# Performance work log

Measured on AMD Instinct MI355X. Metric: run time of the kernel, lower is better.

Reference implementation:

```python
import jax, jax.numpy as jnp
import numpy as np

N, E, IN, HID, ADIM, EDIM, H = 20000, 320000, 128, 128, 16, 16, 2


def _lin(key, out_d, in_d, scale=0.05):
    kw, kb = jax.random.split(key)
    W = jax.random.normal(kw, (out_d, in_d), jnp.float32) * scale
    b = jax.random.normal(kb, (out_d,), jnp.float32) * scale
    return W, b


def _gat_params(key):
    k = jax.random.split(key, 4)
    Wl, bl = _lin(k[0], H * HID, HID)
    Wr, br = _lin(k[1], H * HID, HID)
    We = jax.random.normal(k[2], (H * HID, EDIM), jnp.float32) * 0.05  # lin_edge, no bias
    att = jax.random.normal(k[3], (1, H, HID), jnp.float32) * 0.05
    bias = jnp.zeros((HID,), jnp.float32)  # concat=False -> out bias of size HID
    return Wl, bl, Wr, br, We, att, bias


def setup_inputs() -> dict:
    key = jax.random.key(0)
    ks = jax.random.split(key, 16)
    inp = {}
    inp['x'] = jax.random.normal(ks[0], (N, IN), jnp.float32)
    inp['edge_index'] = jax.random.randint(ks[1], (2, E), 0, N, jnp.int64 if jax.config.jax_enable_x64 else jnp.int32)
    inp['edge_attr'] = jax.random.normal(ks[2], (E, EDIM), jnp.float32)
    inp['action'] = jax.random.normal(ks[3], (N, ADIM), jnp.float32)
    inp['inp_W'], inp['inp_b'] = _lin(ks[4], HID, IN)
    for i, name in enumerate(['s1', 's2', 'sa']):
        Wl, bl, Wr, br, We, att, bias = _gat_params(ks[5 + i])
        inp[f'{name}_Wl'], inp[f'{name}_bl'] = Wl, bl
        inp[f'{name}_Wr'], inp[f'{name}_br'] = Wr, br
        inp[f'{name}_We'], inp[f'{name}_att'], inp[f'{name}_bias'] = We, att, bias
    inp['ap_W'], inp['ap_b'] = _lin(ks[8], HID, ADIM)
    inp['g_W'], inp['g_b'] = _lin(ks[9], HID, HID)
    inp['be_W'], inp['be_b'] = _lin(ks[10], HID, HID)
    inp['q1_W'], inp['q1_b'] = _lin(ks[11], HID, HID)
    inp['q2_W'], inp['q2_b'] = _lin(ks[12], 1, HID)
    return inp


def gatv2(h, src, dst, ea, Wl, bl, Wr, br, We, att, bias):
    """PyG GATv2Conv, heads=H, concat=False (mean over heads), with edge_attr."""
    n = h.shape[0]
    xl = (h @ Wl.T + bl).reshape(n, H, HID)   # source transform
    xr = (h @ Wr.T + br).reshape(n, H, HID)   # destination transform
    em = (ea @ We.T).reshape(-1, H, HID)      # [E,H,C]
    m = jax.nn.leaky_relu(xl[src] + xr[dst] + em, 0.2)   # [E,H,C]
    logit = (m * att).sum(-1)                 # [E,H]
    lmax = jax.ops.segment_max(logit, dst, num_segments=n)
    w = jnp.exp(logit - lmax[dst])
    den = jax.ops.segment_sum(w, dst, num_segments=n)
    alpha = w / den[dst]                      # segment softmax over incoming edges
    out = jax.ops.segment_sum(alpha[..., None] * xl[src], dst, num_segments=n)  # [n,H,C]
    return out.mean(axis=1) + bias


def reference(x, edge_index, edge_attr, action, inp_W, inp_b,
              s1_Wl, s1_bl, s1_Wr, s1_br, s1_We, s1_att, s1_bias,
              s2_Wl, s2_bl, s2_Wr, s2_br, s2_We, s2_att, s2_bias,
              sa_Wl, sa_bl, sa_Wr, sa_br, sa_We, sa_att, sa_bias,
              ap_W, ap_b, g_W, g_b, be_W, be_b, q1_W, q1_b, q2_W, q2_b):
    src, dst = edge_index[0], edge_index[1]
    h = jax.nn.relu(x @ inp_W.T + inp_b)
    h = jax.nn.relu(gatv2(h, src, dst, edge_attr, s1_Wl, s1_bl, s1_Wr, s1_br, s1_We, s1_att, s1_bias))
    h = jax.nn.relu(gatv2(h, src, dst, edge_attr, s2_Wl, s2_bl, s2_Wr, s2_br, s2_We, s2_att, s2_bias))
    a = jax.nn.relu(action @ ap_W.T + ap_b)
    h = (a @ g_W.T + g_b) * h + (a @ be_W.T + be_b)   # FiLM modulation
    h = jax.nn.relu(gatv2(h, src, dst, edge_attr, sa_Wl, sa_bl, sa_Wr, sa_br, sa_We, sa_att, sa_bias))
    h = jax.nn.relu(h @ q1_W.T + q1_b)
    q_node = h @ q2_W.T + q2_b                         # [N,1]
    return q_node.mean(axis=0, keepdims=True)          # [1,1]
```

## Files before the change

### kernel.cpp

```cpp
#include <hip/hip_runtime.h>
#include <hip/hip_bf16.h>


typedef __attribute__((ext_vector_type(8))) short bf16x8;
typedef __attribute__((ext_vector_type(4))) float f32x4;
typedef __attribute__((ext_vector_type(2))) float f32x2;

#define ZERO8 ((bf16x8){0, 0, 0, 0, 0, 0, 0, 0})

__device__ __forceinline__ unsigned short f2bf(float f) {
    union { float f; unsigned int i; } v; v.f = f;
    unsigned int x = v.i;
    x += 0x7fffu + ((x >> 16) & 1u);
    return (unsigned short)(x >> 16);
}
__device__ __forceinline__ unsigned char f2fp8(float f) {
    return (unsigned char)(__builtin_amdgcn_cvt_pk_fp8_f32(f, f, 0, false) & 0xFF);
}
__device__ __forceinline__ void wave_lds_fence() {
    __builtin_amdgcn_wave_barrier();
    asm volatile("s_waitcnt lgkmcnt(0)" ::: "memory");
    __builtin_amdgcn_wave_barrier();
}

#define MAXCVT 16
struct CvtDescs {
    const float* src[MAXCVT];
    unsigned short* dst[MAXCVT];
    int off4[MAXCVT + 1];
    int cnt;
    int* deg; int ndeg4;
    int* ctr; float* col;
};
__global__ __launch_bounds__(256) void cvt_many_kernel(CvtDescs d) {
    const int tid = blockIdx.x * blockDim.x + threadIdx.x;
    const int stride = gridDim.x * blockDim.x;
    const int total = d.off4[d.cnt];
    for (int i = tid; i < total; i += stride) {
        int e = 0;
        while (d.off4[e + 1] <= i) ++e;
        const int j = i - d.off4[e];
        float4 v = ((const float4*)d.src[e])[j];
        ((ushort4*)d.dst[e])[j] = make_ushort4(f2bf(v.x), f2bf(v.y), f2bf(v.z), f2bf(v.w));
    }
    for (int i = tid; i < d.ndeg4; i += stride)
        ((int4*)d.deg)[i] = make_int4(0, 0, 0, 0);
    if (tid == 0) { *d.ctr = 0; *d.col = 0.f; }
}

__global__ void hist_kernel(const int* __restrict__ dst, int* __restrict__ deg, int n) {
    int i = blockIdx.x * blockDim.x + threadIdx.x;
    if (i < n) atomicAdd(&deg[dst[i]], 1);
}

__global__ __launch_bounds__(1024) void scan_kernel(const int* __restrict__ deg,
                                                    int* __restrict__ rowp,
                                                    int* __restrict__ cur, int n) {
    __shared__ int sums[1024];
    const int t = threadIdx.x;
    const int PER = 20;
    int base = t * PER;
    int local[PER];
    int run = 0;
#pragma unroll
    for (int i = 0; i < PER; ++i) {
        int v = (base + i < n) ? deg[base + i] : 0;
        local[i] = run; run += v;
    }
    sums[t] = run; __syncthreads();
    for (int off = 1; off < 1024; off <<= 1) {
        int v = (t >= off) ? sums[t - off] : 0;
        __syncthreads();
        sums[t] += v;
        __syncthreads();
    }
    int offs = (t > 0) ? sums[t - 1] : 0;
#pragma unroll
    for (int i = 0; i < PER; ++i) {
        int idx = base + i;
        if (idx < n) { int v = offs + local[i]; rowp[idx] = v; cur[idx] = v; }
    }
    if (t == 0) rowp[n] = sums[1023];
}

__global__ void scatter_kernel(const int* __restrict__ src, const int* __restrict__ dst,
                               int* __restrict__ cur, const float4* __restrict__ ea,
                               int* __restrict__ csrs, int* __restrict__ csrd,
                               ushort4* __restrict__ eacsr, int n) {
    int i = blockIdx.x * blockDim.x + threadIdx.x;
    if (i < n) {
        int d = dst[i];
        int p = atomicAdd(&cur[d], 1);
        csrs[p] = src[i];
        csrd[p] = d;
        const float4* er = ea + (size_t)i * 4;
        ushort4* eo = eacsr + (size_t)p * 4;
#pragma unroll
        for (int q = 0; q < 4; ++q) {
            float4 v = er[q];
            eo[q] = make_ushort4(f2bf(v.x), f2bf(v.y), f2bf(v.z), f2bf(v.w));
        }
    }
}

template <bool RELU, bool SPLIT, bool AF32>
__global__ __launch_bounds__(256) void gemm_mfma_kernel(
    const void* __restrict__ Ap, const unsigned short* __restrict__ W,
    const float* __restrict__ bias0, const float* __restrict__ bias1, int bsplit,
    unsigned short* __restrict__ Cbf, unsigned char* __restrict__ Cf8,
    int M, int N, int K) {
    __shared__ unsigned char ctile[SPLIT ? 128 * 64 : 64];
    const int t = threadIdx.x;
    const int wave = t >> 6, lane = t & 63;
    const int lo = lane & 15, quad = lane >> 4;
    const int m0 = blockIdx.y * 128 + wave * 32;
    const int n0 = blockIdx.x * 64;

    f32x4 acc[2][4];
#pragma unroll
    for (int i = 0; i < 2; ++i)
#pragma unroll
        for (int j = 0; j < 4; ++j) acc[i][j] = (f32x4){0.f, 0.f, 0.f, 0.f};

    for (int k0 = 0; k0 < K; k0 += 32) {
        bf16x8 af[2], bfr[4];
#pragma unroll
        for (int mi = 0; mi < 2; ++mi) {
            const int mb = m0 + mi * 16;
            if (mb >= M) { af[mi] = ZERO8; continue; }
            if (AF32) {
                const float* A = (const float*)Ap;
                float4 a0 = *(const float4*)(A + (size_t)(mb + lo) * K + k0 + quad * 8);
                float4 a1 = *(const float4*)(A + (size_t)(mb + lo) * K + k0 + quad * 8 + 4);
                bf16x8 f;
                f[0] = (short)f2bf(a0.x); f[1] = (short)f2bf(a0.y);
                f[2] = (short)f2bf(a0.z); f[3] = (short)f2bf(a0.w);
                f[4] = (short)f2bf(a1.x); f[5] = (short)f2bf(a1.y);
                f[6] = (short)f2bf(a1.z); f[7] = (short)f2bf(a1.w);
                af[mi] = f;
            } else {
                const unsigned short* A = (const unsigned short*)Ap;
                af[mi] = *(const bf16x8*)(A + (size_t)(mb + lo) * K + k0 + quad * 8);
            }
        }
#pragma unroll
        for (int ni = 0; ni < 4; ++ni)
            bfr[ni] = *(const bf16x8*)(W + (size_t)(n0 + ni * 16 + lo) * K + k0 + quad * 8);
#pragma unroll
        for (int mi = 0; mi < 2; ++mi)
#pragma unroll
            for (int ni = 0; ni < 4; ++ni)
                acc[mi][ni] = __builtin_amdgcn_mfma_f32_16x16x32_bf16(af[mi], bfr[ni], acc[mi][ni], 0, 0, 0);
    }

    float bn[4];
#pragma unroll
    for (int ni = 0; ni < 4; ++ni) {
        const int n = n0 + ni * 16 + lo;
        const float* bp = (n < bsplit) ? bias0 : bias1;
        const int bi = (n < bsplit) ? n : n - bsplit;
        bn[ni] = bp[bi];
    }
    if (SPLIT) {
#pragma unroll
        for (int mi = 0; mi < 2; ++mi) {
#pragma unroll
            for (int ni = 0; ni < 4; ++ni) {
                const int n = ni * 16 + lo;
#pragma unroll
                for (int r = 0; r < 4; ++r) {
                    float o = acc[mi][ni][r] + bn[ni];
                    if (RELU) o = fmaxf(o, 0.f);
                    ctile[(wave * 32 + mi * 16 + quad * 4 + r) * 64 + n] = f2fp8(o);
                }
            }
        }
        __syncthreads();
        const int row = t >> 1, half = t & 1;
        const int grow = blockIdx.y * 128 + row;
        if (grow < M) {
            const unsigned char* srcp = &ctile[row * 64 + half * 32];
            unsigned char* dstp = Cf8 + (size_t)grow * 512 + n0 + half * 32;
            *(int4*)(dstp) = *(const int4*)(srcp);
            *(int4*)(dstp + 16) = *(const int4*)(srcp + 16);
        }
    } else {
#pragma unroll
        for (int mi = 0; mi < 2; ++mi) {
            const int mb = m0 + mi * 16;
            if (mb >= M) continue;
#pragma unroll
            for (int ni = 0; ni < 4; ++ni) {
                const int n = n0 + ni * 16 + lo;
#pragma unroll
                for (int r = 0; r < 4; ++r) {
                    float o = acc[mi][ni][r] + bn[ni];
                    if (RELU) o = fmaxf(o, 0.f);
                    Cbf[(size_t)(mb + quad * 4 + r) * N + n] = f2bf(o);
                }
            }
        }
    }
}

__global__ __launch_bounds__(256) void gemm_film_kernel(
    const unsigned short* __restrict__ A, const unsigned short* __restrict__ Wg,
    const unsigned short* __restrict__ Wb, const float* __restrict__ gb,
    const float* __restrict__ bb, unsigned short* __restrict__ hbf, int M) {
    const int K = 128, N = 128;
    const int t = threadIdx.x;
    const int wave = t >> 6, lane = t & 63;
    const int lo = lane & 15, quad = lane >> 4;
    const int m0 = blockIdx.y * 128 + wave * 32;
    const int n0 = blockIdx.x * 64;

    f32x4 accg[2][4], accb[2][4];
#pragma unroll
    for (int i = 0; i < 2; ++i)
#pragma unroll
        for (int j = 0; j < 4; ++j) { accg[i][j] = (f32x4){0.f,0.f,0.f,0.f}; accb[i][j] = accg[i][j]; }

    for (int k0 = 0; k0 < 128; k0 += 32) {
        bf16x8 af[2], bg4[4];
#pragma unroll
        for (int mi = 0; mi < 2; ++mi) {
            const int mb = m0 + mi * 16;
            af[mi] = (mb < M) ? *(const bf16x8*)(A + (size_t)(mb + lo) * K + k0 + quad * 8)
                              : ZERO8;
        }
#pragma unroll
        for (int ni = 0; ni < 4; ++ni)
            bg4[ni] = *(const bf16x8*)(Wg + (size_t)(n0 + ni * 16 + lo) * K + k0 + quad * 8);
#pragma unroll
        for (int mi = 0; mi < 2; ++mi)
#pragma unroll
            for (int ni = 0; ni < 4; ++ni)
                accg[mi][ni] = __builtin_amdgcn_mfma_f32_16x16x32_bf16(af[mi], bg4[ni], accg[mi][ni], 0, 0, 0);
#pragma unroll
        for (int ni = 0; ni < 4; ++ni)
            bg4[ni] = *(const bf16x8*)(Wb + (size_t)(n0 + ni * 16 + lo) * K + k0 + quad * 8);
#pragma unroll
        for (int mi = 0; mi < 2; ++mi)
#pragma unroll
            for (int ni = 0; ni < 4; ++ni)
                accb[mi][ni] = __builtin_amdgcn_mfma_f32_16x16x32_bf16(af[mi], bg4[ni], accb[mi][ni], 0, 0, 0);
    }

#pragma unroll
    for (int mi = 0; mi < 2; ++mi) {
        const int mb = m0 + mi * 16;
        if (mb >= M) continue;
#pragma unroll
        for (int ni = 0; ni < 4; ++ni) {
            const int n = n0 + ni * 16 + lo;
            const float g = gb[n], b = bb[n];
#pragma unroll
            for (int r = 0; r < 4; ++r) {
                const size_t idx = (size_t)(mb + quad * 4 + r) * N + n;
                union { unsigned int i; float f; } hv; hv.i = (unsigned int)hbf[idx] << 16;
                hbf[idx] = f2bf((accg[mi][ni][r] + g) * hv.f + (accb[mi][ni][r] + b));
            }
        }
    }
}

__global__ __launch_bounds__(256) void gemm_q1_kernel(
    const unsigned short* __restrict__ A, const unsigned short* __restrict__ W,
    const float* __restrict__ q1b, const float* __restrict__ q2w,
    const float* __restrict__ q2b, float* __restrict__ outsum,
    float* __restrict__ outv, int* __restrict__ ctr,
    int M, int nblk, float invn) {
    const int K = 128;
    const int t = threadIdx.x;
    const int wave = t >> 6, lane = t & 63;
    const int lo = lane & 15, quad = lane >> 4;
    const int m0 = blockIdx.y * 128 + wave * 32;
    const int n0 = blockIdx.x * 64;
    __shared__ float red[4];

    f32x4 acc[2][4];
#pragma unroll
    for (int i = 0; i < 2; ++i)
#pragma unroll
        for (int j = 0; j < 4; ++j) acc[i][j] = (f32x4){0.f, 0.f, 0.f, 0.f};

    for (int k0 = 0; k0 < K; k0 += 32) {
        bf16x8 af[2], bfr[4];
#pragma unroll
        for (int mi = 0; mi < 2; ++mi) {
            const int mb = m0 + mi * 16;
            af[mi] = (mb < M) ? *(const bf16x8*)(A + (size_t)(mb + lo) * K + k0 + quad * 8)
                              : ZERO8;
        }
#pragma unroll
        for (int ni = 0; ni < 4; ++ni)
            bfr[ni] = *(const bf16x8*)(W + (size_t)(n0 + ni * 16 + lo) * K + k0 + quad * 8);
#pragma unroll
        for (int mi = 0; mi < 2; ++mi)
#pragma unroll
            for (int ni = 0; ni < 4; ++ni)
                acc[mi][ni] = __builtin_amdgcn_mfma_f32_16x16x32_bf16(af[mi], bfr[ni], acc[mi][ni], 0, 0, 0);
    }

    float partial = 0.f;
#pragma unroll
    for (int mi = 0; mi < 2; ++mi) {
        const int mb = m0 + mi * 16;
        if (mb >= M) continue;
#pragma unroll
        for (int ni = 0; ni < 4; ++ni) {
            const int n = n0 + ni * 16 + lo;
            const float b = q1b[n], w = q2w[n];
#pragma unroll
            for (int r = 0; r < 4; ++r)
                partial += fmaxf(acc[mi][ni][r] + b, 0.f) * w;
        }
    }
    partial += __shfl_xor(partial, 1);  partial += __shfl_xor(partial, 2);
    partial += __shfl_xor(partial, 4);  partial += __shfl_xor(partial, 8);
    partial += __shfl_xor(partial, 16); partial += __shfl_xor(partial, 32);
    if (lane == 0) red[wave] = partial;
    __syncthreads();
    if (t == 0) {
        atomicAdd(outsum, red[0] + red[1] + red[2] + red[3]);
        __threadfence();
        unsigned int d = atomicAdd((unsigned int*)ctr, 1u);
        if (d == (unsigned int)(nblk - 1)) {
            float s = atomicAdd(outsum, 0.f);
            outv[0] = s * invn + q2b[0];
        }
    }
}

template <int BK, bool RELU>
__global__ __launch_bounds__(256) void gemm_kernel(const float* __restrict__ A,
                                                   const float* __restrict__ W,
                                                   const float* __restrict__ bp,
                                                   unsigned short* __restrict__ Cbf,
                                                   int M, int N, int K) {
    __shared__ float As[BK][68];
    __shared__ float Ws[BK][68];
    const int t = threadIdx.x;
    const int m0 = blockIdx.y * 64;
    const int n0 = blockIdx.x * 64;
    const int tx = t & 15, ty = t >> 4;
    float acc[4][4];
#pragma unroll
    for (int i = 0; i < 4; ++i)
#pragma unroll
        for (int j = 0; j < 4; ++j) acc[i][j] = 0.f;

    for (int k0 = 0; k0 < K; k0 += BK) {
        const int r = t >> 2, cc = (t & 3) * 4;
        const int arow = m0 + r;
        float4 av = (arow < M) ? *(const float4*)(A + (size_t)arow * K + k0 + cc)
                               : make_float4(0.f, 0.f, 0.f, 0.f);
        As[cc + 0][r] = av.x; As[cc + 1][r] = av.y;
        As[cc + 2][r] = av.z; As[cc + 3][r] = av.w;
        float4 wv = *(const float4*)(W + (size_t)(n0 + r) * K + k0 + cc);
        Ws[cc + 0][r] = wv.x; Ws[cc + 1][r] = wv.y;
        Ws[cc + 2][r] = wv.z; Ws[cc + 3][r] = wv.w;
        __syncthreads();
#pragma unroll
        for (int k = 0; k < BK; ++k) {
            float4 a4 = *(const float4*)&As[k][ty * 4];
            float4 b4 = *(const float4*)&Ws[k][tx * 4];
            float a_[4] = {a4.x, a4.y, a4.z, a4.w};
            float b_[4] = {b4.x, b4.y, b4.z, b4.w};
#pragma unroll
            for (int i = 0; i < 4; ++i)
#pragma unroll
                for (int j = 0; j < 4; ++j) acc[i][j] += a_[i] * b_[j];
        }
        __syncthreads();
    }
    float4 bj = *(const float4*)(bp + n0 + tx * 4);
    float bb[4] = {bj.x, bj.y, bj.z, bj.w};
#pragma unroll
    for (int i = 0; i < 4; ++i) {
        int row = m0 + ty * 4 + i;
        if (row < M) {
            float o[4];
#pragma unroll
            for (int j = 0; j < 4; ++j) {
                o[j] = acc[i][j] + bb[j];
                if (RELU) o[j] = fmaxf(o[j], 0.f);
            }
            *(ushort4*)(Cbf + (size_t)row * N + n0 + tx * 4) =
                make_ushort4(f2bf(o[0]), f2bf(o[1]), f2bf(o[2]), f2bf(o[3]));
        }
    }
}

#define LSTR 272
__global__ __launch_bounds__(256, 4) void gat_logit_kernel(
    const unsigned char* __restrict__ xf8,
    const int* __restrict__ csrs, const int* __restrict__ csrd,
    const unsigned short* __restrict__ eacsr, const unsigned short* __restrict__ we16,
    const float* __restrict__ att, float* __restrict__ logit, int E) {
    __shared__ float attl[256];
    __shared__ __align__(16) unsigned char xls[4][16 * LSTR];
    __shared__ __align__(16) unsigned char xrs[4][16 * LSTR];
    const int tid = threadIdx.x;
    attl[tid] = att[tid];
    const int wave = tid >> 6, lane = tid & 63;
    const int lo = lane & 15, quad = lane >> 4;
    const int sr_row = lane >> 2, c16 = (lane & 3) * 16;

    bf16x8 wef[16];
#pragma unroll
    for (int t = 0; t < 16; ++t)
        wef[t] = (quad < 2) ? *(const bf16x8*)(we16 + (size_t)(t * 16 + lo) * 16 + quad * 8)
                            : ZERO8;
    __syncthreads();

    const int nb = (E + 15) / 16;
    const int wstride = gridDim.x * 4;
    const int trips = (nb + wstride - 1) / wstride;
    for (int it = 0; it < trips; ++it) {
        const int b = blockIdx.x * 4 + wave + it * wstride;
        if (b >= nb) break;
        const int p0 = b * 16;
        {
            const int pr = min(p0 + sr_row, E - 1);
            const int sr = csrs[pr], dr = csrd[pr];
            const unsigned char* xs = xf8 + (size_t)sr * 512 + c16;
            const unsigned char* xrp = xf8 + (size_t)dr * 512 + 256 + c16;
            unsigned char* ld = &xls[wave][sr_row * LSTR + c16];
            unsigned char* rd = &xrs[wave][sr_row * LSTR + c16];
#pragma unroll
            for (int j = 0; j < 4; ++j) {
                *(int4*)(ld + j * 64) = *(const int4*)(xs + j * 64);
                *(int4*)(rd + j * 64) = *(const int4*)(xrp + j * 64);
            }
        }
        wave_lds_fence();
        {
            const bool valid = (p0 + lo) < E;
            const int p = valid ? (p0 + lo) : (E - 1);
            const bf16x8 eaf = (quad < 2)
                ? *(const bf16x8*)(eacsr + (size_t)p * 16 + quad * 8) : ZERO8;
            float ph0 = 0.f, ph1 = 0.f;
#pragma unroll
            for (int t = 0; t < 16; ++t) {
                f32x4 D = __builtin_amdgcn_mfma_f32_16x16x32_bf16(
                    wef[t], eaf, (f32x4){0.f, 0.f, 0.f, 0.f}, 0, 0, 0);
                const int c0 = t * 16 + quad * 4;
                const unsigned int xlu = *(const unsigned int*)&xls[wave][lo * LSTR + c0];
                const unsigned int xru = *(const unsigned int*)&xrs[wave][lo * LSTR + c0];
                const f32x2 l01 = __builtin_amdgcn_cvt_pk_f32_fp8(xlu, false);
                const f32x2 l23 = __builtin_amdgcn_cvt_pk_f32_fp8(xlu, true);
                const f32x2 r01 = __builtin_amdgcn_cvt_pk_f32_fp8(xru, false);
                const f32x2 r23 = __builtin_amdgcn_cvt_pk_f32_fp8(xru, true);
                const float4 at4 = *(const float4*)&attl[c0];
                float vx = l01.x + r01.x + D[0];
                float vy = l01.y + r01.y + D[1];
                float vz = l23.x + r23.x + D[2];
                float vw = l23.y + r23.y + D[3];
                vx = fmaxf(vx, 0.2f * vx); vy = fmaxf(vy, 0.2f * vy);
                vz = fmaxf(vz, 0.2f * vz); vw = fmaxf(vw, 0.2f * vw);
                const float pt = vx * at4.x + vy * at4.y + vz * at4.z + vw * at4.w;
                if (t < 8) ph0 += pt; else ph1 += pt;
            }
            ph0 += __shfl_xor(ph0, 16); ph0 += __shfl_xor(ph0, 32);
            ph1 += __shfl_xor(ph1, 16); ph1 += __shfl_xor(ph1, 32);
            if (valid) {
                if (quad == 0) logit[p0 + lo] = __expf(fminf(ph0, 60.f));
                else if (quad == 1) logit[(size_t)E + p0 + lo] = __expf(fminf(ph1, 60.f));
            }
        }
        wave_lds_fence();
    }
}

__global__ __launch_bounds__(256) void gat_na_kernel(
    const unsigned char* __restrict__ xf8,
    const int* __restrict__ rowp, const int* __restrict__ csrs,
    const float* __restrict__ wgt, const float* __restrict__ bias,
    unsigned short* __restrict__ houtb, int nnodes, int E) {
    const int lane = threadIdx.x & 63;
    const int node = blockIdx.x * 4 + (threadIdx.x >> 6);
    if (node >= nnodes) return;
    const int rs = rowp[node], re = rowp[node + 1];
    const int h = lane >> 5;
    const float* lg = wgt + (size_t)h * E;

    float den = 0.f;
    float4 acc = make_float4(0.f, 0.f, 0.f, 0.f);
    int i = rs;
    for (; i + 3 < re; i += 4) {
        const int s0 = csrs[i], s1 = csrs[i + 1], s2 = csrs[i + 2], s3 = csrs[i + 3];
        const float w0 = lg[i], w1 = lg[i + 1], w2 = lg[i + 2], w3 = lg[i + 3];
        const unsigned int u0 = *(const unsigned int*)(xf8 + (size_t)s0 * 512 + 4 * lane);
        const unsigned int u1 = *(const unsigned int*)(xf8 + (size_t)s1 * 512 + 4 * lane);
        const unsigned int u2 = *(const unsigned int*)(xf8 + (size_t)s2 * 512 + 4 * lane);
        const unsigned int u3 = *(const unsigned int*)(xf8 + (size_t)s3 * 512 + 4 * lane);
        den += (w0 + w1) + (w2 + w3);
        f32x2 p01, p23;
        p01 = __builtin_amdgcn_cvt_pk_f32_fp8(u0, false);
        p23 = __builtin_amdgcn_cvt_pk_f32_fp8(u0, true);
        acc.x += w0 * p01.x; acc.y += w0 * p01.y; acc.z += w0 * p23.x; acc.w += w0 * p23.y;
        p01 = __builtin_amdgcn_cvt_pk_f32_fp8(u1, false);
        p23 = __builtin_amdgcn_cvt_pk_f32_fp8(u1, true);
        acc.x += w1 * p01.x; acc.y += w1 * p01.y; acc.z += w1 * p23.x; acc.w += w1 * p23.y;
        p01 = __builtin_amdgcn_cvt_pk_f32_fp8(u2, false);
        p23 = __builtin_amdgcn_cvt_pk_f32_fp8(u2, true);
        acc.x += w2 * p01.x; acc.y += w2 * p01.y; acc.z += w2 * p23.x; acc.w += w2 * p23.y;
        p01 = __builtin_amdgcn_cvt_pk_f32_fp8(u3, false);
        p23 = __builtin_amdgcn_cvt_pk_f32_fp8(u3, true);
        acc.x += w3 * p01.x; acc.y += w3 * p01.y; acc.z += w3 * p23.x; acc.w += w3 * p23.y;
    }
    for (; i < re; ++i) {
        const int s0 = csrs[i];
        const float w0 = lg[i];
        const unsigned int u0 = *(const unsigned int*)(xf8 + (size_t)s0 * 512 + 4 * lane);
        const f32x2 p01 = __builtin_amdgcn_cvt_pk_f32_fp8(u0, false);
        const f32x2 p23 = __builtin_amdgcn_cvt_pk_f32_fp8(u0, true);
        den += w0;
        acc.x += w0 * p01.x; acc.y += w0 * p01.y; acc.z += w0 * p23.x; acc.w += w0 * p23.y;
    }
    const float inv = (re > rs) ? 1.f / den : 0.f;
    float ox = acc.x * inv, oy = acc.y * inv, oz = acc.z * inv, ow = acc.w * inv;
    ox += __shfl_xor(ox, 32); oy += __shfl_xor(oy, 32);
    oz += __shfl_xor(oz, 32); ow += __shfl_xor(ow, 32);
    if (lane < 32) {
        float4 bu = *(const float4*)(bias + 4 * lane);
        *(ushort4*)(houtb + (size_t)node * 128 + 4 * lane) = make_ushort4(
            f2bf(fmaxf(0.5f * ox + bu.x, 0.f)), f2bf(fmaxf(0.5f * oy + bu.y, 0.f)),
            f2bf(fmaxf(0.5f * oz + bu.z, 0.f)), f2bf(fmaxf(0.5f * ow + bu.w, 0.f)));
    }
}

extern "C" void kernel_launch(void* const* d_in, const int* in_sizes, int n_in,
                              void* d_out, int out_size, void* d_ws, size_t ws_size,
                              hipStream_t stream) {
    const int N = in_sizes[0] / 128;
    const int E = in_sizes[1] / 2;

    typedef const float* fp;
    fp x      = (fp)d_in[0];
    const int* ei = (const int*)d_in[1];
    fp ea     = (fp)d_in[2];
    fp action = (fp)d_in[3];
    fp inp_W  = (fp)d_in[4];
    fp inp_b  = (fp)d_in[5];
    fp ap_W = (fp)d_in[27], ap_b = (fp)d_in[28];
    fp g_W  = (fp)d_in[29], g_b  = (fp)d_in[30];
    fp be_W = (fp)d_in[31], be_b = (fp)d_in[32];
    fp q1_W = (fp)d_in[33], q1_b = (fp)d_in[34];
    fp q2_W = (fp)d_in[35], q2_b = (fp)d_in[36];

    char* base = (char*)d_ws;
    size_t off = 0;
    auto alloc = [&](size_t bytes) { char* p = base + off; off = (off + bytes + 255) & ~(size_t)255; return p; };
    unsigned char*  xf8 = (unsigned char*)alloc((size_t)N * 512);
    float* col  = (float*)alloc(128 * 4);
    int* ctr    = (int*)alloc(256);
    int* deg    = (int*)alloc((size_t)N * 4);
    int* rowp   = (int*)alloc((size_t)(N + 1) * 4);
    int* cur    = (int*)alloc((size_t)N * 4);
    int* csrs   = (int*)alloc((size_t)E * 4);
    int* csrd   = (int*)alloc((size_t)E * 4);
    unsigned short* eacsr = (unsigned short*)alloc((size_t)E * 16 * 2);
    float* wgt  = (float*)alloc((size_t)2 * E * 4);
    unsigned short* hbf = (unsigned short*)alloc((size_t)N * 128 * 2);
    unsigned short* abf = (unsigned short*)alloc((size_t)N * 128 * 2);
    unsigned short* wbf = (unsigned short*)alloc((262144 + 3 * 4096) * 2);
    (void)ws_size; (void)n_in; (void)out_size;

    unsigned short* winp = wbf;
    unsigned short* w1l  = wbf + 16384;
    unsigned short* w1r  = w1l + 32768;
    unsigned short* w2l  = w1r + 32768;
    unsigned short* w2r  = w2l + 32768;
    unsigned short* wal  = w2r + 32768;
    unsigned short* war  = wal + 32768;
    unsigned short* wg   = war + 32768;
    unsigned short* wbe  = wg + 16384;
    unsigned short* wq1  = wbe + 16384;
    unsigned short* wep1 = wq1 + 16384;
    unsigned short* wep2 = wep1 + 4096;
    unsigned short* wep3 = wep2 + 4096;

    const int* src = ei;
    const int* dst = ei + E;

    CvtDescs cd;
    int ce = 0, acc4 = 0;
    auto addc = [&](const float* s, unsigned short* d, int n) {
        cd.src[ce] = s; cd.dst[ce] = d; cd.off4[ce] = acc4; acc4 += n / 4; ++ce; };
    addc(inp_W, winp, 16384);
    addc((fp)d_in[6],  w1l, 32768); addc((fp)d_in[8],  w1r, 32768);
    addc((fp)d_in[13], w2l, 32768); addc((fp)d_in[15], w2r, 32768);
    addc((fp)d_in[20], wal, 32768); addc((fp)d_in[22], war, 32768);
    addc(g_W, wg, 16384); addc(be_W, wbe, 16384); addc(q1_W, wq1, 16384);
    addc((fp)d_in[10], wep1, 4096); addc((fp)d_in[17], wep2, 4096); addc((fp)d_in[24], wep3, 4096);
    cd.off4[ce] = acc4; cd.cnt = ce;
    cd.deg = deg; cd.ndeg4 = (N + 3) / 4;
    cd.ctr = ctr; cd.col = col;
    cvt_many_kernel<<<(acc4 + 255) / 256, 256, 0, stream>>>(cd);

    hist_kernel<<<(E + 255) / 256, 256, 0, stream>>>(dst, deg, E);
    scan_kernel<<<1, 1024, 0, stream>>>(deg, rowp, cur, N);
    scatter_kernel<<<(E + 255) / 256, 256, 0, stream>>>(src, dst, cur, (const float4*)ea,
                                                        csrs, csrd, (ushort4*)eacsr, E);

    const int my = (N + 127) / 128;
    const int nodeg = (N + 3) / 4;

    auto run_gat = [&](const unsigned short* wep, const float* at, const float* bi,
                       unsigned short* hb) {
        gat_logit_kernel<<<2500, 256, 0, stream>>>(xf8, csrs, csrd, eacsr, wep, at, wgt, E);
        gat_na_kernel<<<nodeg, 256, 0, stream>>>(xf8, rowp, csrs, wgt, bi, hb, N, E);
    };

    gemm_mfma_kernel<true, false, true><<<dim3(2, my), 256, 0, stream>>>(
        x, winp, inp_b, inp_b, 128, hbf, nullptr, N, 128, 128);

    gemm_mfma_kernel<false, true, false><<<dim3(8, my), 256, 0, stream>>>(
        hbf, w1l, (fp)d_in[7], (fp)d_in[9], 256, nullptr, xf8, N, 512, 128);
    run_gat(wep1, (fp)d_in[11], (fp)d_in[12], hbf);
    gemm_mfma_kernel<false, true, false><<<dim3(8, my), 256, 0, stream>>>(
        hbf, w2l, (fp)d_in[14], (fp)d_in[16], 256, nullptr, xf8, N, 512, 128);
    run_gat(wep2, (fp)d_in[18], (fp)d_in[19], hbf);

    gemm_kernel<16, true><<<dim3(2, (N + 63) / 64), 256, 0, stream>>>(
        action, ap_W, ap_b, abf, N, 128, 16);
    gemm_film_kernel<<<dim3(2, my), 256, 0, stream>>>(abf, wg, wbe, g_b, be_b, hbf, N);

    gemm_mfma_kernel<false, true, false><<<dim3(8, my), 256, 0, stream>>>(
        hbf, wal, (fp)d_in[21], (fp)d_in[23], 256, nullptr, xf8, N, 512, 128);
    run_gat(wep3, (fp)d_in[25], (fp)d_in[26], hbf);

    gemm_q1_kernel<<<dim3(2, my), 256, 0, stream>>>(
        hbf, wq1, q1_b, q2_W, q2_b, col, (float*)d_out, ctr, N, 2 * my, 1.0f / (float)N);
}
```

Measured before the change: 423.1 us.

## Fuse GATv2 logit and neighbor aggregation into one per-node kernel

Replaces the edge-parallel logit kernel and the node-parallel aggregation kernel with a single kernel in which each wave owns one destination node. It walks that node's CSR edges in chunks of 16, computing the exp-logits with MFMA and reusing the gathered source features already staged in LDS for the weighted sum. The intent is to avoid writing and re-reading the per-edge logit array, to drop the csrd array, to load the destination features once per node instead of per edge, and to gather each source row only once. The trade-offs are wasted MFMA lanes on partial chunks for low-degree nodes, load imbalance across skewed degrees, and reloading the edge-weight fragments in every one of many small blocks.

```diff
diff --git a/kernel.cpp b/kernel.cpp
--- a/kernel.cpp
+++ b/kernel.cpp
@@ -85,14 +85,13 @@
 
 __global__ void scatter_kernel(const int* __restrict__ src, const int* __restrict__ dst,
                                int* __restrict__ cur, const float4* __restrict__ ea,
-                               int* __restrict__ csrs, int* __restrict__ csrd,
+                               int* __restrict__ csrs,
                                ushort4* __restrict__ eacsr, int n) {
     int i = blockIdx.x * blockDim.x + threadIdx.x;
     if (i < n) {
         int d = dst[i];
         int p = atomicAdd(&cur[d], 1);
         csrs[p] = src[i];
-        csrd[p] = d;
         const float4* er = ea + (size_t)i * 4;
         ushort4* eo = eacsr + (size_t)p * 4;
 #pragma unroll
@@ -393,14 +392,16 @@
 }
 
 #define LSTR 272
-__global__ __launch_bounds__(256, 4) void gat_logit_kernel(
+__global__ __launch_bounds__(256, 4) void gat_fused_kernel(
     const unsigned char* __restrict__ xf8,
-    const int* __restrict__ csrs, const int* __restrict__ csrd,
+    const int* __restrict__ rowp, const int* __restrict__ csrs,
     const unsigned short* __restrict__ eacsr, const unsigned short* __restrict__ we16,
-    const float* __restrict__ att, float* __restrict__ logit, int E) {
+    const float* __restrict__ att, const float* __restrict__ bias,
+    unsigned short* __restrict__ houtb, int nnodes) {
     __shared__ float attl[256];
     __shared__ __align__(16) unsigned char xls[4][16 * LSTR];
-    __shared__ __align__(16) unsigned char xrs[4][16 * LSTR];
+    __shared__ __align__(16) unsigned char xrs[4][256];
+    __shared__ float wls[4][2][16];
     const int tid = threadIdx.x;
     attl[tid] = att[tid];
     const int wave = tid >> 6, lane = tid & 63;
@@ -414,30 +415,31 @@
                             : ZERO8;
     __syncthreads();
 
-    const int nb = (E + 15) / 16;
-    const int wstride = gridDim.x * 4;
-    const int trips = (nb + wstride - 1) / wstride;
-    for (int it = 0; it < trips; ++it) {
-        const int b = blockIdx.x * 4 + wave + it * wstride;
-        if (b >= nb) break;
-        const int p0 = b * 16;
+    const int node = blockIdx.x * 4 + wave;
+    if (node >= nnodes) return;
+    const int rs = rowp[node], re = rowp[node + 1];
+
+    *(unsigned int*)&xrs[wave][4 * lane] =
+        *(const unsigned int*)(xf8 + (size_t)node * 512 + 256 + 4 * lane);
+
+    const int h = lane >> 5;
+    float den = 0.f;
+    float4 acc = make_float4(0.f, 0.f, 0.f, 0.f);
+
+    for (int cb = rs; cb < re; cb += 16) {
         {
-            const int pr = min(p0 + sr_row, E - 1);
-            const int sr = csrs[pr], dr = csrd[pr];
+            const int pr = min(cb + sr_row, re - 1);
+            const int sr = csrs[pr];
             const unsigned char* xs = xf8 + (size_t)sr * 512 + c16;
-            const unsigned char* xrp = xf8 + (size_t)dr * 512 + 256 + c16;
             unsigned char* ld = &xls[wave][sr_row * LSTR + c16];
-            unsigned char* rd = &xrs[wave][sr_row * LSTR + c16];
-#pragma unroll
-            for (int j = 0; j < 4; ++j) {
+#pragma unroll
+            for (int j = 0; j < 4; ++j)
                 *(int4*)(ld + j * 64) = *(const int4*)(xs + j * 64);
-                *(int4*)(rd + j * 64) = *(const int4*)(xrp + j * 64);
-            }
         }
         wave_lds_fence();
         {
-            const bool valid = (p0 + lo) < E;
-            const int p = valid ? (p0 + lo) : (E - 1);
+            const bool valid = (cb + lo) < re;
+            const int p = valid ? (cb + lo) : (re - 1);
             const bf16x8 eaf = (quad < 2)
                 ? *(const bf16x8*)(eacsr + (size_t)p * 16 + quad * 8) : ZERO8;
             float ph0 = 0.f, ph1 = 0.f;
@@ -447,7 +449,7 @@
                     wef[t], eaf, (f32x4){0.f, 0.f, 0.f, 0.f}, 0, 0, 0);
                 const int c0 = t * 16 + quad * 4;
                 const unsigned int xlu = *(const unsigned int*)&xls[wave][lo * LSTR + c0];
-                const unsigned int xru = *(const unsigned int*)&xrs[wave][lo * LSTR + c0];
+                const unsigned int xru = *(const unsigned int*)&xrs[wave][c0];
                 const f32x2 l01 = __builtin_amdgcn_cvt_pk_f32_fp8(xlu, false);
                 const f32x2 l23 = __builtin_amdgcn_cvt_pk_f32_fp8(xlu, true);
                 const f32x2 r01 = __builtin_amdgcn_cvt_pk_f32_fp8(xru, false);
@@ -464,61 +466,27 @@
             }
             ph0 += __shfl_xor(ph0, 16); ph0 += __shfl_xor(ph0, 32);
             ph1 += __shfl_xor(ph1, 16); ph1 += __shfl_xor(ph1, 32);
-            if (valid) {
-                if (quad == 0) logit[p0 + lo] = __expf(fminf(ph0, 60.f));
-                else if (quad == 1) logit[(size_t)E + p0 + lo] = __expf(fminf(ph1, 60.f));
+            if (quad == 0) {
+                wls[wave][0][lo] = valid ? __expf(fminf(ph0, 60.f)) : 0.f;
+                wls[wave][1][lo] = valid ? __expf(fminf(ph1, 60.f)) : 0.f;
             }
         }
         wave_lds_fence();
-    }
-}
-
-__global__ __launch_bounds__(256) void gat_na_kernel(
-    const unsigned char* __restrict__ xf8,
-    const int* __restrict__ rowp, const int* __restrict__ csrs,
-    const float* __restrict__ wgt, const float* __restrict__ bias,
-    unsigned short* __restrict__ houtb, int nnodes, int E) {
-    const int lane = threadIdx.x & 63;
-    const int node = blockIdx.x * 4 + (threadIdx.x >> 6);
-    if (node >= nnodes) return;
-    const int rs = rowp[node], re = rowp[node + 1];
-    const int h = lane >> 5;
-    const float* lg = wgt + (size_t)h * E;
-
-    float den = 0.f;
-    float4 acc = make_float4(0.f, 0.f, 0.f, 0.f);
-    int i = rs;
-    for (; i + 3 < re; i += 4) {
-        const int s0 = csrs[i], s1 = csrs[i + 1], s2 = csrs[i + 2], s3 = csrs[i + 3];
-        const float w0 = lg[i], w1 = lg[i + 1], w2 = lg[i + 2], w3 = lg[i + 3];
-        const unsigned int u0 = *(const unsigned int*)(xf8 + (size_t)s0 * 512 + 4 * lane);
-        const unsigned int u1 = *(const unsigned int*)(xf8 + (size_t)s1 * 512 + 4 * lane);
-        const unsigned int u2 = *(const unsigned int*)(xf8 + (size_t)s2 * 512 + 4 * lane);
-        const unsigned int u3 = *(const unsigned int*)(xf8 + (size_t)s3 * 512 + 4 * lane);
-        den += (w0 + w1) + (w2 + w3);
-        f32x2 p01, p23;
-        p01 = __builtin_amdgcn_cvt_pk_f32_fp8(u0, false);
-        p23 = __builtin_amdgcn_cvt_pk_f32_fp8(u0, true);
-        acc.x += w0 * p01.x; acc.y += w0 * p01.y; acc.z += w0 * p23.x; acc.w += w0 * p23.y;
-        p01 = __builtin_amdgcn_cvt_pk_f32_fp8(u1, false);
-        p23 = __builtin_amdgcn_cvt_pk_f32_fp8(u1, true);
-        acc.x += w1 * p01.x; acc.y += w1 * p01.y; acc.z += w1 * p23.x; acc.w += w1 * p23.y;
-        p01 = __builtin_amdgcn_cvt_pk_f32_fp8(u2, false);
-        p23 = __builtin_amdgcn_cvt_pk_f32_fp8(u2, true);
-        acc.x += w2 * p01.x; acc.y += w2 * p01.y; acc.z += w2 * p23.x; acc.w += w2 * p23.y;
-        p01 = __builtin_amdgcn_cvt_pk_f32_fp8(u3, false);
-        p23 = __builtin_amdgcn_cvt_pk_f32_fp8(u3, true);
-        acc.x += w3 * p01.x; acc.y += w3 * p01.y; acc.z += w3 * p23.x; acc.w += w3 * p23.y;
-    }
-    for (; i < re; ++i) {
-        const int s0 = csrs[i];
-        const float w0 = lg[i];
-        const unsigned int u0 = *(const unsigned int*)(xf8 + (size_t)s0 * 512 + 4 * lane);
-        const f32x2 p01 = __builtin_amdgcn_cvt_pk_f32_fp8(u0, false);
-        const f32x2 p23 = __builtin_amdgcn_cvt_pk_f32_fp8(u0, true);
-        den += w0;
-        acc.x += w0 * p01.x; acc.y += w0 * p01.y; acc.z += w0 * p23.x; acc.w += w0 * p23.y;
-    }
+        {
+            const int ne = min(16, re - cb);
+            for (int e = 0; e < ne; ++e) {
+                const float w = wls[wave][h][e];
+                const unsigned int u = *(const unsigned int*)&xls[wave][e * LSTR + 4 * lane];
+                const f32x2 p01 = __builtin_amdgcn_cvt_pk_f32_fp8(u, false);
+                const f32x2 p23 = __builtin_amdgcn_cvt_pk_f32_fp8(u, true);
+                den += w;
+                acc.x += w * p01.x; acc.y += w * p01.y;
+                acc.z += w * p23.x; acc.w += w * p23.y;
+            }
+        }
+        wave_lds_fence();
+    }
+
     const float inv = (re > rs) ? 1.f / den : 0.f;
     float ox = acc.x * inv, oy = acc.y * inv, oz = acc.z * inv, ow = acc.w * inv;
     ox += __shfl_xor(ox, 32); oy += __shfl_xor(oy, 32);
@@ -560,9 +528,7 @@
     int* rowp   = (int*)alloc((size_t)(N + 1) * 4);
     int* cur    = (int*)alloc((size_t)N * 4);
     int* csrs   = (int*)alloc((size_t)E * 4);
-    int* csrd   = (int*)alloc((size_t)E * 4);
     unsigned short* eacsr = (unsigned short*)alloc((size_t)E * 16 * 2);
-    float* wgt  = (float*)alloc((size_t)2 * E * 4);
     unsigned short* hbf = (unsigned short*)alloc((size_t)N * 128 * 2);
     unsigned short* abf = (unsigned short*)alloc((size_t)N * 128 * 2);
     unsigned short* wbf = (unsigned short*)alloc((262144 + 3 * 4096) * 2);
@@ -603,15 +569,14 @@
     hist_kernel<<<(E + 255) / 256, 256, 0, stream>>>(dst, deg, E);
     scan_kernel<<<1, 1024, 0, stream>>>(deg, rowp, cur, N);
     scatter_kernel<<<(E + 255) / 256, 256, 0, stream>>>(src, dst, cur, (const float4*)ea,
-                                                        csrs, csrd, (ushort4*)eacsr, E);
+                                                        csrs, (ushort4*)eacsr, E);
 
     const int my = (N + 127) / 128;
     const int nodeg = (N + 3) / 4;
 
     auto run_gat = [&](const unsigned short* wep, const float* at, const float* bi,
                        unsigned short* hb) {
-        gat_logit_kernel<<<2500, 256, 0, stream>>>(xf8, csrs, csrd, eacsr, wep, at, wgt, E);
-        gat_na_kernel<<<nodeg, 256, 0, stream>>>(xf8, rowp, csrs, wgt, bi, hb, N, E);
+        gat_fused_kernel<<<nodeg, 256, 0, stream>>>(xf8, rowp, csrs, eacsr, wep, at, bi, hb, N);
     };
 
     gemm_mfma_kernel<true, false, true><<<dim3(2, my), 256, 0, stream>>>(
```

After: 436.6 us. 1.03x slower.
